# Kernel tuning notes

Measured on AMD Instinct MI355X. Metric: run time of the kernel, lower is better.

Reference implementation:

```python
import jax, jax.numpy as jnp
import numpy as np

M_IND = 1024   # inducing points
K_NN = 16      # nearest neighbors
JITTER = 1e-4


def rbf(X, Z):
    # unit-variance, unit-lengthscale RBF kernel; returns (K, squared distances)
    sq = jnp.sum(X * X, -1)[:, None] + jnp.sum(Z * Z, -1)[None, :] - 2.0 * (X @ Z.T)
    sq = jnp.maximum(sq, 0.0)
    return jnp.exp(-0.5 * sq), sq


def setup_inputs() -> dict:
    key = jax.random.key(0)
    k1, k2, k3 = jax.random.split(key, 3)
    return {
        "X": jax.random.normal(k1, (65536, 3), jnp.float32),
        "Z": jax.random.normal(k2, (M_IND, 3), jnp.float32),
        "Lu_raw": jax.random.normal(k3, (M_IND, M_IND), jnp.float32),
        "mu": jnp.zeros((M_IND,), jnp.float32),
    }


def reference(X, Z, Lu_raw, mu):
    N = X.shape[0]
    Kxx = jnp.ones((N,), X.dtype)                      # diag of RBF(X,X) is 1
    Kxz, dist = rbf(X, Z)                              # [N,M], [N,M]
    Kzz, _ = rbf(Z, Z)                                 # [M,M]

    # transform_to(lower_cholesky): strict lower triangle + exp(diag)
    Lu = jnp.tril(Lu_raw, -1) + jnp.diag(jnp.exp(jnp.diag(Lu_raw)))

    eyeM = jnp.eye(M_IND, dtype=X.dtype)
    L = jnp.linalg.cholesky(Kzz + JITTER * eyeM)       # [M,M]
    Kzz_j = L @ L.T                                    # == little_L @ little_L.T math (Kzz + jitter*I)
    Su = Lu @ Lu.T                                     # full variational covariance

    # K nearest inducing points per data point (argsort(dist)[:, :K])
    _, idx = jax.lax.top_k(-dist, K_NN)                # [N,K]

    lKzz = Kzz_j[idx[:, :, None], idx[:, None, :]]     # [N,K,K] gathered submatrices
    lS = Su[idx[:, :, None], idx[:, None, :]]          # [N,K,K]
    lKxz = jnp.take_along_axis(Kxz, idx, axis=1)       # [N,K]
    lmu = mu[idx]                                      # [N,K]

    eyeK = jnp.eye(K_NN, dtype=X.dtype)
    inv = jnp.linalg.inv(lKzz + JITTER * eyeK)         # batched tiny inverses [N,K,K]
    W = jnp.einsum('nk,nkj->nj', lKxz, inv)            # [N,K]

    mean = jnp.einsum('nk,nk->n', W, lmu)              # [N]
    cov = (Kxx
           - jnp.einsum('ni,nij,nj->n', W, lKzz, W)
           + jnp.einsum('ni,nij,nj->n', W, lS, W))
    std = jnp.sqrt(jnp.clip(cov, 0.05, None))          # qF scale = clamp(cov, 0.05)**0.5
    return jnp.stack([mean, std])                      # [2,N] qF parameters
```

## Files before the change

### kernel.cpp

```cpp
#include <hip/hip_runtime.h>
#include <math.h>

#define N_PTS 65536
#define M_IND 1024
#define KNN 16
#define JITTER 1e-4f

#define PACKED_FLOATS (M_IND * (M_IND + 1) / 2)
#define PACKED_BYTES  ((size_t)PACKED_FLOATS * sizeof(float))

#define TSU 32
#define SU_BLOCKS 528
#define PTS_PER_BLK 128
#define QSTRIDE 17
#define GRID_BLKS (N_PTS / PTS_PER_BLK)


__device__ __forceinline__ void su_tile(const float* __restrict__ Lu_raw,
                                        float* __restrict__ P,
                                        int bid, int tid,
                                        float (*As)[36], float (*Bs)[36]) {
    int rt = (int)((sqrtf(8.0f * (float)bid + 1.0f) - 1.0f) * 0.5f);
    while ((rt + 1) * (rt + 2) / 2 <= bid) ++rt;
    while (rt * (rt + 1) / 2 > bid) --rt;
    int ct = bid - rt * (rt + 1) / 2;
    int i0 = rt * TSU, j0 = ct * TSU;

    int tx = tid & 15, ty = tid >> 4;
    int sr = tid >> 3, sc = (tid & 7) << 2;
    float a00 = 0.f, a01 = 0.f, a10 = 0.f, a11 = 0.f;

    int nch = ct + 1;
    int gi = i0 + sr, gj = j0 + sr;
    float4 pa = *(const float4*)(Lu_raw + (unsigned)gi * M_IND + sc);
    float4 pb = *(const float4*)(Lu_raw + (unsigned)gj * M_IND + sc);

    for (int c = 0; c < nch; ++c) {
        int gk = (c << 5) + sc;
        float aa[4] = {pa.x, pa.y, pa.z, pa.w};
        float bb[4] = {pb.x, pb.y, pb.z, pb.w};
        #pragma unroll
        for (int q = 0; q < 4; ++q) {
            int k = gk + q;
            aa[q] = (k < gi) ? aa[q] : ((k == gi) ? __expf(aa[q]) : 0.0f);
            bb[q] = (k < gj) ? bb[q] : ((k == gj) ? __expf(bb[q]) : 0.0f);
        }
        *(float4*)&As[sr][sc] = make_float4(aa[0], aa[1], aa[2], aa[3]);
        *(float4*)&Bs[sr][sc] = make_float4(bb[0], bb[1], bb[2], bb[3]);
        __syncthreads();
        if (c + 1 < nch) {
            int kn = ((c + 1) << 5) + sc;
            pa = *(const float4*)(Lu_raw + (unsigned)gi * M_IND + kn);
            pb = *(const float4*)(Lu_raw + (unsigned)gj * M_IND + kn);
        }
        #pragma unroll
        for (int kk = 0; kk < 32; kk += 4) {
            float4 av0 = *(const float4*)&As[ty][kk];
            float4 av1 = *(const float4*)&As[ty + 16][kk];
            float4 bv0 = *(const float4*)&Bs[tx][kk];
            float4 bv1 = *(const float4*)&Bs[tx + 16][kk];
            a00 = fmaf(av0.x, bv0.x, fmaf(av0.y, bv0.y, fmaf(av0.z, bv0.z, fmaf(av0.w, bv0.w, a00))));
            a01 = fmaf(av0.x, bv1.x, fmaf(av0.y, bv1.y, fmaf(av0.z, bv1.z, fmaf(av0.w, bv1.w, a01))));
            a10 = fmaf(av1.x, bv0.x, fmaf(av1.y, bv0.y, fmaf(av1.z, bv0.z, fmaf(av1.w, bv0.w, a10))));
            a11 = fmaf(av1.x, bv1.x, fmaf(av1.y, bv1.y, fmaf(av1.z, bv1.z, fmaf(av1.w, bv1.w, a11))));
        }
        __syncthreads();
    }

    int ia = i0 + ty, ib = i0 + ty + 16;
    int ja = j0 + tx, jb = j0 + tx + 16;
    if (ja <= ia) P[((unsigned)ia * (ia + 1) >> 1) + ja] = a00;
    if (jb <= ia) P[((unsigned)ia * (ia + 1) >> 1) + jb] = a01;
    if (ja <= ib) P[((unsigned)ib * (ib + 1) >> 1) + ja] = a10;
    if (jb <= ib) P[((unsigned)ib * (ib + 1) >> 1) + jb] = a11;
}

__global__ __launch_bounds__(256) void su_kernel(const float* __restrict__ Lu_raw,
                                                 float* __restrict__ P) {
    __shared__ float As[TSU][36];
    __shared__ float Bs[TSU][36];
    su_tile(Lu_raw, P, blockIdx.x, threadIdx.x, As, Bs);
}

__device__ __forceinline__ void ce(unsigned long long& x, unsigned long long& y) {
    unsigned long long a = x, b = y;
    bool c = a < b;
    x = c ? a : b;
    y = c ? b : a;
}
__device__ __forceinline__ void ce(float& x, float& y) {
    float a = fminf(x, y), b = fmaxf(x, y);
    x = a; y = b;
}

template <typename KT>
__device__ __forceinline__ void sort16(KT* a) {
    #pragma unroll
    for (int p = 1; p < 16; p <<= 1)
        #pragma unroll
        for (int k = p; k >= 1; k >>= 1)
            #pragma unroll
            for (int j = k & (p - 1); j + k < 16; j += 2 * k)
                #pragma unroll
                for (int i = 0; i < k; ++i)
                    if (i + j + k < 16)
                        if (((i + j) / (2 * p)) == ((i + j + k) / (2 * p)))
                            ce(a[i + j], a[i + j + k]);
}

template <typename KT>
__device__ __forceinline__ void cleanup16(KT* a) {
    #pragma unroll
    for (int d = 8; d >= 1; d >>= 1)
        #pragma unroll
        for (int i = 0; i < 16; ++i)
            if ((i & d) == 0) ce(a[i], a[i | d]);
}

__device__ __forceinline__ float uval(float4 z, float xn0, float xn1, float xn2) {
    return fmaf(xn0, z.x, fmaf(xn1, z.y, fmaf(xn2, z.z, z.w)));
}

template <int MODE>
__global__ __launch_bounds__(256, 2) void vnngp_kernel(const float* __restrict__ X,
                                                       const float* __restrict__ Z,
                                                       const float* __restrict__ mu,
                                                       float* __restrict__ P,
                                                       const float* __restrict__ Lu_raw,
                                                       unsigned int* __restrict__ ctr,
                                                       float* __restrict__ out) {
    __shared__ __align__(16) char smem[37888];
    float4* Zs = (float4*)smem;
    float* mus = (float*)(smem + 16384);
    unsigned long long* qb = (unsigned long long*)(smem + 20480);
    int tid = threadIdx.x;

    for (int r = tid; r < M_IND; r += 256) {
        float zx = Z[r * 3 + 0], zy = Z[r * 3 + 1], zz = Z[r * 3 + 2];
        Zs[r] = make_float4(zx, zy, zz, 0.5f * (zx * zx + zy * zy + zz * zz));
        mus[r] = mu[r];
    }

    if (MODE == 2) {
        float (*As)[36] = (float (*)[36])(smem + 20480);
        float (*Bs)[36] = (float (*)[36])(smem + 20480 + 4608);
        int t = blockIdx.x;
        #pragma unroll
        for (int r = 16; r < 32; ++r) {
            int s = (r * (r + 1)) >> 1;
            if (t >= s) ++t;
        }
        su_tile(Lu_raw, P, t, tid, As, Bs);
        if (blockIdx.x < 16) {
            int r = 16 + blockIdx.x;
            su_tile(Lu_raw, P, (r * (r + 1)) >> 1, tid, As, Bs);
        }
        __syncthreads();
        if (tid == 0) {
            __threadfence();
            atomicAdd(ctr, 1u);
        }
    } else {
        __syncthreads();
    }

    {
        int pt = tid >> 2, sub = tid & 3;
        int nA = blockIdx.x * PTS_PER_BLK + pt;
        int nB = nA + 64;
        float xA0 = X[nA * 3 + 0], xA1 = X[nA * 3 + 1], xA2 = X[nA * 3 + 2];
        float xB0 = X[nB * 3 + 0], xB1 = X[nB * 3 + 1], xB2 = X[nB * 3 + 2];
        float xqA = fmaf(xA0, xA0, fmaf(xA1, xA1, xA2 * xA2));
        float xqB = fmaf(xB0, xB0, fmaf(xB1, xB1, xB2 * xB2));
        float nA0 = -xA0, nA1 = -xA1, nA2 = -xA2;
        float nB0 = -xB0, nB1 = -xB1, nB2 = -xB2;
        int mbase = sub << 8;
        int rot = sub << 1;

        float TA[16], TB[16];
        #pragma unroll
        for (int j = 0; j < 16; ++j) { TA[j] = 3.4e38f; TB[j] = 3.4e38f; }
        #pragma unroll 1
        for (int c = 0; c < 16; ++c) {
            int base = mbase + (c << 4);
            #pragma unroll
            for (int j = 0; j < 16; ++j) {
                int m = base + ((j + rot) & 15);
                float4 z = Zs[m];
                TA[j] = fminf(TA[j], uval(z, nA0, nA1, nA2));
                TB[j] = fminf(TB[j], uval(z, nB0, nB1, nB2));
            }
        }
        sort16(TA);
        sort16(TB);
        #pragma unroll
        for (int round = 1; round <= 2; round <<= 1) {
            float oA[16], oB[16];
            #pragma unroll
            for (int i = 0; i < 16; ++i) {
                oA[i] = __shfl_xor(TA[i], round, 64);
                oB[i] = __shfl_xor(TB[i], round, 64);
            }
            #pragma unroll
            for (int i = 0; i < 16; ++i) {
                TA[i] = fminf(TA[i], oA[15 - i]);
                TB[i] = fminf(TB[i], oB[15 - i]);
            }
            cleanup16(TA);
            cleanup16(TB);
        }
        float TstarA = TA[15], TstarB = TB[15];

        unsigned short* mycA = ((unsigned short*)qb) + pt * (QSTRIDE * 4) + sub * 16;
        unsigned short* mycB = ((unsigned short*)qb) + (pt + 64) * (QSTRIDE * 4) + sub * 16;
        int cntA = 0, cntB = 0;
        #pragma unroll 1
        for (int c = 0; c < 16; ++c) {
            int base = mbase + (c << 4);
            #pragma unroll
            for (int j = 0; j < 16; ++j) {
                int m = base + ((j + rot) & 15);
                float4 z = Zs[m];
                float uA = uval(z, nA0, nA1, nA2);
                float uB = uval(z, nB0, nB1, nB2);
                if (uA <= TstarA) { if (cntA < 16) mycA[cntA] = (unsigned short)m; ++cntA; }
                if (uB <= TstarB) { if (cntB < 16) mycB[cntB] = (unsigned short)m; ++cntB; }
            }
        }

        int ovfA = cntA > 16 ? 1 : 0;
        ovfA |= __shfl_xor(ovfA, 1, 64);
        ovfA |= __shfl_xor(ovfA, 2, 64);
        int ovfB = cntB > 16 ? 1 : 0;
        ovfB |= __shfl_xor(ovfB, 1, 64);
        ovfB |= __shfl_xor(ovfB, 2, 64);

        if (!ovfA) {
            const unsigned long long* m64 = (const unsigned long long*)mycA;
            unsigned long long raw[4] = {m64[0], m64[1], m64[2], m64[3]};
            unsigned long long C[16];
            #pragma unroll
            for (int i = 0; i < 16; ++i) {
                int m = (int)((raw[i >> 2] >> ((i & 3) * 16)) & 0x3FF);
                float u = uval(Zs[m], nA0, nA1, nA2);
                float d = fmaxf(fmaf(2.0f, u, xqA), 0.0f);
                unsigned long long key =
                    ((unsigned long long)__float_as_uint(d) << 32) | (unsigned)m;
                C[i] = (i < cntA) ? key : ~0ULL;
            }
            sort16(C);
            #pragma unroll
            for (int round = 1; round <= 2; round <<= 1) {
                unsigned long long o[16];
                #pragma unroll
                for (int i = 0; i < 16; ++i) o[i] = __shfl_xor(C[i], round, 64);
                #pragma unroll
                for (int i = 0; i < 16; ++i) {
                    unsigned long long b = o[15 - i];
                    C[i] = C[i] < b ? C[i] : b;
                }
                cleanup16(C);
            }
            if (sub == 0) {
                #pragma unroll
                for (int i = 0; i < 16; ++i) qb[pt * QSTRIDE + i] = C[i];
            }
        } else if (sub == 0) {
            unsigned long long R[16];
            #pragma unroll
            for (int i = 0; i < 16; ++i) R[i] = ~0ULL;
            for (int m = 0; m < M_IND; ++m) {
                float u = uval(Zs[m], nA0, nA1, nA2);
                float d = fmaxf(fmaf(2.0f, u, xqA), 0.0f);
                unsigned long long kk =
                    ((unsigned long long)__float_as_uint(d) << 32) | (unsigned)m;
                if (kk < R[15]) {
                    #pragma unroll
                    for (int j = 0; j < 16; ++j) {
                        unsigned long long t = R[j];
                        bool cc = kk < t;
                        R[j] = cc ? kk : t;
                        kk = cc ? t : kk;
                    }
                }
            }
            #pragma unroll
            for (int i = 0; i < 16; ++i) qb[pt * QSTRIDE + i] = R[i];
        }

        if (!ovfB) {
            const unsigned long long* m64 = (const unsigned long long*)mycB;
            unsigned long long raw[4] = {m64[0], m64[1], m64[2], m64[3]};
            unsigned long long C[16];
            #pragma unroll
            for (int i = 0; i < 16; ++i) {
                int m = (int)((raw[i >> 2] >> ((i & 3) * 16)) & 0x3FF);
                float u = uval(Zs[m], nB0, nB1, nB2);
                float d = fmaxf(fmaf(2.0f, u, xqB), 0.0f);
                unsigned long long key =
                    ((unsigned long long)__float_as_uint(d) << 32) | (unsigned)m;
                C[i] = (i < cntB) ? key : ~0ULL;
            }
            sort16(C);
            #pragma unroll
            for (int round = 1; round <= 2; round <<= 1) {
                unsigned long long o[16];
                #pragma unroll
                for (int i = 0; i < 16; ++i) o[i] = __shfl_xor(C[i], round, 64);
                #pragma unroll
                for (int i = 0; i < 16; ++i) {
                    unsigned long long b = o[15 - i];
                    C[i] = C[i] < b ? C[i] : b;
                }
                cleanup16(C);
            }
            if (sub == 0) {
                #pragma unroll
                for (int i = 0; i < 16; ++i) qb[(pt + 64) * QSTRIDE + i] = C[i];
            }
        } else if (sub == 0) {
            unsigned long long R[16];
            #pragma unroll
            for (int i = 0; i < 16; ++i) R[i] = ~0ULL;
            for (int m = 0; m < M_IND; ++m) {
                float u = uval(Zs[m], nB0, nB1, nB2);
                float d = fmaxf(fmaf(2.0f, u, xqB), 0.0f);
                unsigned long long kk =
                    ((unsigned long long)__float_as_uint(d) << 32) | (unsigned)m;
                if (kk < R[15]) {
                    #pragma unroll
                    for (int j = 0; j < 16; ++j) {
                        unsigned long long t = R[j];
                        bool cc = kk < t;
                        R[j] = cc ? kk : t;
                        kk = cc ? t : kk;
                    }
                }
            }
            #pragma unroll
            for (int i = 0; i < 16; ++i) qb[(pt + 64) * QSTRIDE + i] = R[i];
        }
    }
    __syncthreads();

    if (MODE == 2) {
        if (tid == 0) {
            while (__hip_atomic_load(ctr, __ATOMIC_ACQUIRE, __HIP_MEMORY_SCOPE_AGENT)
                   < (unsigned)GRID_BLKS)
                __builtin_amdgcn_s_sleep(8);
        }
        __syncthreads();
    }
    if (tid >= PTS_PER_BLK) return;

    int n = blockIdx.x * PTS_PER_BLK + tid;
    int idx[KNN];
    float kv[KNN];
    float nx[KNN], ny[KNN], nz[KNN], nq[KNN];
    #pragma unroll
    for (int a = 0; a < KNN; ++a) {
        unsigned long long k = qb[tid * QSTRIDE + a];
        idx[a] = (int)(k & 0xFFFFFFFFULL);
        float d = __uint_as_float((unsigned)(k >> 32));
        kv[a] = __expf(-0.5f * d);
        float4 z = Zs[idx[a]];
        nx[a] = z.x; ny[a] = z.y; nz[a] = z.z; nq[a] = z.w;
    }

    float A[KNN * (KNN + 1) / 2];
    #pragma unroll
    for (int r = 0; r < KNN; ++r) {
        A[r * (r + 1) / 2 + r] = 1.0f + 2.0f * JITTER;
        #pragma unroll
        for (int c = 0; c < r; ++c) {
            float dot = fmaf(nx[r], nx[c], fmaf(ny[r], ny[c], nz[r] * nz[c]));
            A[r * (r + 1) / 2 + c] = __expf(fminf(dot - nq[r] - nq[c], 0.0f));
        }
    }

    #pragma unroll
    for (int c = 0; c < KNN; ++c) {
        float diag = A[c * (c + 1) / 2 + c];
        #pragma unroll
        for (int k = 0; k < c; ++k) {
            float l = A[c * (c + 1) / 2 + k];
            diag = fmaf(-l, l, diag);
        }
        float rinv = __frsqrt_rn(fmaxf(diag, 1e-12f));
        A[c * (c + 1) / 2 + c] = rinv;
        #pragma unroll
        for (int r = c + 1; r < KNN; ++r) {
            float v = A[r * (r + 1) / 2 + c];
            #pragma unroll
            for (int k = 0; k < c; ++k)
                v = fmaf(-A[r * (r + 1) / 2 + k], A[c * (c + 1) / 2 + k], v);
            A[r * (r + 1) / 2 + c] = v * rinv;
        }
    }

    float w[KNN];
    #pragma unroll
    for (int r = 0; r < KNN; ++r) {
        float v = kv[r];
        #pragma unroll
        for (int c = 0; c < r; ++c) v = fmaf(-A[r * (r + 1) / 2 + c], w[c], v);
        w[r] = v * A[r * (r + 1) / 2 + r];
    }
    #pragma unroll
    for (int r = KNN - 1; r >= 0; --r) {
        float v = w[r];
        #pragma unroll
        for (int c = r + 1; c < KNN; ++c) v = fmaf(-A[c * (c + 1) / 2 + r], w[c], v);
        w[r] = v * A[r * (r + 1) / 2 + r];
    }

    float wk = 0.f, ww = 0.f, mean = 0.f;
    #pragma unroll
    for (int a = 0; a < KNN; ++a) {
        wk = fmaf(w[a], kv[a], wk);
        ww = fmaf(w[a], w[a], ww);
        mean = fmaf(w[a], mus[idx[a]], mean);
    }

    float qs = 0.f;
    if (MODE != 0) {
        #pragma unroll
        for (int r = 0; r < KNN; ++r) {
            int a = idx[r];
            float wr = w[r];
            float rowacc = 0.f;
            #pragma unroll
            for (int c = 0; c < r; ++c) {
                int b = idx[c];
                int hi = a > b ? a : b;
                int lo = a > b ? b : a;
                rowacc = fmaf(w[c], P[((unsigned)hi * (hi + 1) >> 1) + lo], rowacc);
            }
            qs = fmaf(wr, fmaf(wr, P[((unsigned)a * (a + 1) >> 1) + a], 2.0f * rowacc), qs);
        }
    } else {
        int si[KNN]; float sw[KNN];
        #pragma unroll
        for (int a = 0; a < KNN; ++a) { si[a] = idx[a]; sw[a] = w[a]; }
        #pragma unroll
        for (int a = 1; a < KNN; ++a) {
            int iv = si[a]; float wv = sw[a];
            int b = a - 1;
            while (b >= 0 && si[b] > iv) { si[b + 1] = si[b]; sw[b + 1] = sw[b]; --b; }
            si[b + 1] = iv; sw[b + 1] = wv;
        }
        int s = 0;
        int kend = si[KNN - 1];
        for (int k = 0; k <= kend; ++k) {
            float v = 0.f;
            if (s < KNN && si[s] == k) {
                v = sw[s] * __expf(Lu_raw[(unsigned)k * M_IND + k]);
                ++s;
            }
            for (int a = s; a < KNN; ++a)
                v = fmaf(sw[a], Lu_raw[(unsigned)si[a] * M_IND + k], v);
            qs = fmaf(v, v, qs);
        }
    }

    float cov = 1.0f - (wk - JITTER * ww) + qs;
    float sd = sqrtf(fmaxf(cov, 0.05f));
    out[n] = mean;
    out[N_PTS + n] = sd;
}

extern "C" void kernel_launch(void* const* d_in, const int* in_sizes, int n_in,
                              void* d_out, int out_size, void* d_ws, size_t ws_size,
                              hipStream_t stream) {
    const float* X      = (const float*)d_in[0];
    const float* Z      = (const float*)d_in[1];
    const float* Lu_raw = (const float*)d_in[2];
    const float* mu     = (const float*)d_in[3];
    float* out = (float*)d_out;

    if (ws_size >= PACKED_BYTES + 64) {
        float* P = (float*)d_ws;
        unsigned int* ctr = (unsigned int*)((char*)d_ws + PACKED_BYTES);
        hipMemsetAsync(ctr, 0, sizeof(unsigned int), stream);
        vnngp_kernel<2><<<GRID_BLKS, 256, 0, stream>>>(X, Z, mu, P, Lu_raw, ctr, out);
    } else if (ws_size >= PACKED_BYTES) {
        float* P = (float*)d_ws;
        su_kernel<<<SU_BLOCKS, 256, 0, stream>>>(Lu_raw, P);
        vnngp_kernel<1><<<GRID_BLKS, 256, 0, stream>>>(X, Z, mu, P, Lu_raw, nullptr, out);
    } else {
        vnngp_kernel<0><<<GRID_BLKS, 256, 0, stream>>>(X, Z, mu, nullptr, Lu_raw, nullptr, out);
    }
}
```

Baseline: 163.0 us.

## Split fused kernel into kNN selection and Cholesky solve kernels via workspace

Adds a two-kernel path used when the workspace is large enough. The first kernel computes the packed Su tiles and a threshold-based top-16 neighbor selection, writing (distance, index) keys to global memory. The second kernel rebuilds the 16x16 Kzz submatrix, solves it with an in-register Cholesky, and splits the Su quadratic form across two threads per point. This removes the global counter synchronisation and the mixed workload of the fused kernel, at the cost of an extra launch and an 8 MB global round trip for the neighbor keys.

Result: slower. 173.8 us (+6.7%).

```diff
diff --git a/kernel.cpp b/kernel.cpp
--- a/kernel.cpp
+++ b/kernel.cpp
@@ -8,6 +8,7 @@
 
 #define PACKED_FLOATS (M_IND * (M_IND + 1) / 2)
 #define PACKED_BYTES  ((size_t)PACKED_FLOATS * sizeof(float))
+#define QBG_BYTES     ((size_t)N_PTS * KNN * 8)
 
 #define TSU 32
 #define SU_BLOCKS 528
@@ -119,6 +120,255 @@
 
 __device__ __forceinline__ float uval(float4 z, float xn0, float xn1, float xn2) {
     return fmaf(xn0, z.x, fmaf(xn1, z.y, fmaf(xn2, z.z, z.w)));
+}
+
+__global__ __launch_bounds__(256, 2) void sel_kernel(const float* __restrict__ X,
+                                                     const float* __restrict__ Z,
+                                                     float* __restrict__ P,
+                                                     const float* __restrict__ Lu_raw,
+                                                     unsigned long long* __restrict__ qbg) {
+    __shared__ __align__(16) char smem[25600];
+    float4* Zs = (float4*)smem;
+    unsigned long long* qb = (unsigned long long*)(smem + 16384);
+    int tid = threadIdx.x;
+
+    for (int r = tid; r < M_IND; r += 256) {
+        float zx = Z[r * 3 + 0], zy = Z[r * 3 + 1], zz = Z[r * 3 + 2];
+        Zs[r] = make_float4(zx, zy, zz, 0.5f * (zx * zx + zy * zy + zz * zz));
+    }
+
+    if (blockIdx.x < SU_BLOCKS) {
+        float (*As)[36] = (float (*)[36])(smem + 16384);
+        float (*Bs)[36] = (float (*)[36])(smem + 16384 + 4608);
+        su_tile(Lu_raw, P, blockIdx.x, tid, As, Bs);
+    } else {
+        __syncthreads();
+    }
+
+    int pt = tid >> 2, sub = tid & 3;
+    int n = blockIdx.x * 64 + pt;
+    float x0 = X[n * 3 + 0], x1 = X[n * 3 + 1], x2 = X[n * 3 + 2];
+    float xq = fmaf(x0, x0, fmaf(x1, x1, x2 * x2));
+    float xn0 = -x0, xn1 = -x1, xn2 = -x2;
+    int mbase = sub << 8;
+    int rot = sub << 1;
+
+    float T[16];
+    #pragma unroll
+    for (int j = 0; j < 16; ++j) T[j] = 3.4e38f;
+    #pragma unroll 1
+    for (int c = 0; c < 16; ++c) {
+        int base = mbase + (c << 4);
+        #pragma unroll
+        for (int j = 0; j < 16; ++j) {
+            int m = base + ((j + rot) & 15);
+            float4 z = Zs[m];
+            T[j] = fminf(T[j], uval(z, xn0, xn1, xn2));
+        }
+    }
+    sort16(T);
+    #pragma unroll
+    for (int round = 1; round <= 2; round <<= 1) {
+        float o[16];
+        #pragma unroll
+        for (int i = 0; i < 16; ++i) o[i] = __shfl_xor(T[i], round, 64);
+        #pragma unroll
+        for (int i = 0; i < 16; ++i) T[i] = fminf(T[i], o[15 - i]);
+        cleanup16(T);
+    }
+    float Tstar = T[15];
+
+    unsigned short* myc = ((unsigned short*)qb) + pt * (QSTRIDE * 4) + sub * 16;
+    int cnt = 0;
+    #pragma unroll 1
+    for (int c = 0; c < 16; ++c) {
+        int base = mbase + (c << 4);
+        #pragma unroll
+        for (int j = 0; j < 16; ++j) {
+            int m = base + ((j + rot) & 15);
+            float4 z = Zs[m];
+            float u = uval(z, xn0, xn1, xn2);
+            if (u <= Tstar) { if (cnt < 16) myc[cnt] = (unsigned short)m; ++cnt; }
+        }
+    }
+
+    int ovf = cnt > 16 ? 1 : 0;
+    ovf |= __shfl_xor(ovf, 1, 64);
+    ovf |= __shfl_xor(ovf, 2, 64);
+
+    unsigned long long* kout = qbg + (size_t)n * KNN;
+
+    if (!ovf) {
+        const unsigned long long* m64 = (const unsigned long long*)myc;
+        unsigned long long raw[4] = {m64[0], m64[1], m64[2], m64[3]};
+        unsigned long long C[16];
+        #pragma unroll
+        for (int i = 0; i < 16; ++i) {
+            int m = (int)((raw[i >> 2] >> ((i & 3) * 16)) & 0x3FF);
+            float u = uval(Zs[m], xn0, xn1, xn2);
+            float d = fmaxf(fmaf(2.0f, u, xq), 0.0f);
+            unsigned long long key =
+                ((unsigned long long)__float_as_uint(d) << 32) | (unsigned)m;
+            C[i] = (i < cnt) ? key : ~0ULL;
+        }
+        sort16(C);
+        #pragma unroll
+        for (int round = 1; round <= 2; round <<= 1) {
+            unsigned long long o[16];
+            #pragma unroll
+            for (int i = 0; i < 16; ++i) o[i] = __shfl_xor(C[i], round, 64);
+            #pragma unroll
+            for (int i = 0; i < 16; ++i) {
+                unsigned long long b = o[15 - i];
+                C[i] = C[i] < b ? C[i] : b;
+            }
+            cleanup16(C);
+        }
+        if (sub == 0) {
+            #pragma unroll
+            for (int i = 0; i < 16; ++i) kout[i] = C[i];
+        }
+    } else if (sub == 0) {
+        unsigned long long R[16];
+        #pragma unroll
+        for (int i = 0; i < 16; ++i) R[i] = ~0ULL;
+        for (int m = 0; m < M_IND; ++m) {
+            float u = uval(Zs[m], xn0, xn1, xn2);
+            float d = fmaxf(fmaf(2.0f, u, xq), 0.0f);
+            unsigned long long kk =
+                ((unsigned long long)__float_as_uint(d) << 32) | (unsigned)m;
+            if (kk < R[15]) {
+                #pragma unroll
+                for (int j = 0; j < 16; ++j) {
+                    unsigned long long t = R[j];
+                    bool cc = kk < t;
+                    R[j] = cc ? kk : t;
+                    kk = cc ? t : kk;
+                }
+            }
+        }
+        #pragma unroll
+        for (int i = 0; i < 16; ++i) kout[i] = R[i];
+    }
+}
+
+__global__ __launch_bounds__(128, 2) void p2_kernel(const float* __restrict__ Z,
+                                                    const float* __restrict__ mu,
+                                                    const float* __restrict__ P,
+                                                    const unsigned long long* __restrict__ qbg,
+                                                    float* __restrict__ out) {
+    __shared__ __align__(16) char smem[20992];
+    float4* Zs = (float4*)smem;
+    float* mus = (float*)(smem + 16384);
+    float* xch = (float*)(smem + 20480);
+    int tid = threadIdx.x;
+
+    for (int r = tid; r < M_IND; r += 128) {
+        float zx = Z[r * 3 + 0], zy = Z[r * 3 + 1], zz = Z[r * 3 + 2];
+        Zs[r] = make_float4(zx, zy, zz, 0.5f * (zx * zx + zy * zy + zz * zz));
+        mus[r] = mu[r];
+    }
+    __syncthreads();
+
+    int role = tid >> 6;
+    int pt = tid & 63;
+    int n = blockIdx.x * 64 + pt;
+
+    int idx[KNN];
+    float kv[KNN];
+    float nx[KNN], ny[KNN], nz[KNN], nq[KNN];
+    const unsigned long long* kp = qbg + (size_t)n * KNN;
+    #pragma unroll
+    for (int a = 0; a < KNN; ++a) {
+        unsigned long long k = kp[a];
+        idx[a] = (int)(k & 0xFFFFFFFFULL);
+        float d = __uint_as_float((unsigned)(k >> 32));
+        kv[a] = __expf(-0.5f * d);
+        float4 z = Zs[idx[a]];
+        nx[a] = z.x; ny[a] = z.y; nz[a] = z.z; nq[a] = z.w;
+    }
+
+    float A[KNN * (KNN + 1) / 2];
+    #pragma unroll
+    for (int r = 0; r < KNN; ++r) {
+        A[r * (r + 1) / 2 + r] = 1.0f + 2.0f * JITTER;
+        #pragma unroll
+        for (int c = 0; c < r; ++c) {
+            float dot = fmaf(nx[r], nx[c], fmaf(ny[r], ny[c], nz[r] * nz[c]));
+            A[r * (r + 1) / 2 + c] = __expf(fminf(dot - nq[r] - nq[c], 0.0f));
+        }
+    }
+
+    #pragma unroll
+    for (int c = 0; c < KNN; ++c) {
+        float diag = A[c * (c + 1) / 2 + c];
+        #pragma unroll
+        for (int k = 0; k < c; ++k) {
+            float l = A[c * (c + 1) / 2 + k];
+            diag = fmaf(-l, l, diag);
+        }
+        float rinv = __frsqrt_rn(fmaxf(diag, 1e-12f));
+        A[c * (c + 1) / 2 + c] = rinv;
+        #pragma unroll
+        for (int r = c + 1; r < KNN; ++r) {
+            float v = A[r * (r + 1) / 2 + c];
+            #pragma unroll
+            for (int k = 0; k < c; ++k)
+                v = fmaf(-A[r * (r + 1) / 2 + k], A[c * (c + 1) / 2 + k], v);
+            A[r * (r + 1) / 2 + c] = v * rinv;
+        }
+    }
+
+    float w[KNN];
+    #pragma unroll
+    for (int r = 0; r < KNN; ++r) {
+        float v = kv[r];
+        #pragma unroll
+        for (int c = 0; c < r; ++c) v = fmaf(-A[r * (r + 1) / 2 + c], w[c], v);
+        w[r] = v * A[r * (r + 1) / 2 + r];
+    }
+    #pragma unroll
+    for (int r = KNN - 1; r >= 0; --r) {
+        float v = w[r];
+        #pragma unroll
+        for (int c = r + 1; c < KNN; ++c) v = fmaf(-A[c * (c + 1) / 2 + r], w[c], v);
+        w[r] = v * A[r * (r + 1) / 2 + r];
+    }
+
+    float wk = 0.f, ww = 0.f, mean = 0.f;
+    #pragma unroll
+    for (int a = 0; a < KNN; ++a) {
+        wk = fmaf(w[a], kv[a], wk);
+        ww = fmaf(w[a], w[a], ww);
+        mean = fmaf(w[a], mus[idx[a]], mean);
+    }
+
+    float qs_p = 0.f;
+    #pragma unroll
+    for (int r = 0; r < KNN; ++r) {
+        if ((r & 1) == role) {
+            int a = idx[r];
+            float wr = w[r];
+            float rowacc = 0.f;
+            #pragma unroll
+            for (int c = 0; c < r; ++c) {
+                int b = idx[c];
+                int hi = a > b ? a : b;
+                int lo = a > b ? b : a;
+                rowacc = fmaf(w[c], P[((unsigned)hi * (hi + 1) >> 1) + lo], rowacc);
+            }
+            qs_p = fmaf(wr, fmaf(wr, P[((unsigned)a * (a + 1) >> 1) + a], 2.0f * rowacc), qs_p);
+        }
+    }
+    xch[tid] = qs_p;
+    __syncthreads();
+    if (role == 0) {
+        float qs = qs_p + xch[tid + 64];
+        float cov = 1.0f - (wk - JITTER * ww) + qs;
+        float sd = sqrtf(fmaxf(cov, 0.05f));
+        out[n] = mean;
+        out[N_PTS + n] = sd;
+    }
 }
 
 template <int MODE>
@@ -478,7 +728,12 @@
     const float* mu     = (const float*)d_in[3];
     float* out = (float*)d_out;
 
-    if (ws_size >= PACKED_BYTES + 64) {
+    if (ws_size >= PACKED_BYTES + QBG_BYTES) {
+        float* P = (float*)d_ws;
+        unsigned long long* qbg = (unsigned long long*)((char*)d_ws + PACKED_BYTES);
+        sel_kernel<<<N_PTS / 64, 256, 0, stream>>>(X, Z, P, Lu_raw, qbg);
+        p2_kernel<<<N_PTS / 64, 128, 0, stream>>>(Z, mu, P, qbg, out);
+    } else if (ws_size >= PACKED_BYTES + 64) {
         float* P = (float*)d_ws;
         unsigned int* ctr = (unsigned int*)((char*)d_ws + PACKED_BYTES);
         hipMemsetAsync(ctr, 0, sizeof(unsigned int), stream);
```

## Split per-point 16x16 Cholesky solve across four lanes with shuffles

Applied to the files above, without the earlier changes.

In the packed-Su modes, each point's 16x16 Cholesky, triangular solves and quadratic form are now spread over a quad of four lanes, each owning four rows in a cyclic layout. Columns and partial sums move between lanes with wavefront shuffles. All 256 threads now do this phase instead of half of them idling, and per-thread register pressure drops. The cost is many shuffle operations and serial dependence through the column loop.

New measurement: 176.0 us. 1.08x slower.

```diff
diff --git a/kernel.cpp b/kernel.cpp
--- a/kernel.cpp
+++ b/kernel.cpp
@@ -120,6 +120,10 @@
 __device__ __forceinline__ float uval(float4 z, float xn0, float xn1, float xn2) {
     return fmaf(xn0, z.x, fmaf(xn1, z.y, fmaf(xn2, z.z, z.w)));
 }
+
+#define LI0(c) ((c) & 3)
+#define LI1(c) ((c) & 7)
+#define LI2(c) ((c) < 12 ? (c) : 0)
 
 template <int MODE>
 __global__ __launch_bounds__(256, 2) void vnngp_kernel(const float* __restrict__ X,
@@ -351,122 +355,299 @@
         }
         __syncthreads();
     }
-    if (tid >= PTS_PER_BLK) return;
-
-    int n = blockIdx.x * PTS_PER_BLK + tid;
-    int idx[KNN];
-    float kv[KNN];
-    float nx[KNN], ny[KNN], nz[KNN], nq[KNN];
-    #pragma unroll
-    for (int a = 0; a < KNN; ++a) {
-        unsigned long long k = qb[tid * QSTRIDE + a];
-        idx[a] = (int)(k & 0xFFFFFFFFULL);
-        float d = __uint_as_float((unsigned)(k >> 32));
-        kv[a] = __expf(-0.5f * d);
-        float4 z = Zs[idx[a]];
-        nx[a] = z.x; ny[a] = z.y; nz[a] = z.z; nq[a] = z.w;
-    }
-
-    float A[KNN * (KNN + 1) / 2];
-    #pragma unroll
-    for (int r = 0; r < KNN; ++r) {
-        A[r * (r + 1) / 2 + r] = 1.0f + 2.0f * JITTER;
-        #pragma unroll
-        for (int c = 0; c < r; ++c) {
-            float dot = fmaf(nx[r], nx[c], fmaf(ny[r], ny[c], nz[r] * nz[c]));
-            A[r * (r + 1) / 2 + c] = __expf(fminf(dot - nq[r] - nq[c], 0.0f));
-        }
-    }
-
-    #pragma unroll
-    for (int c = 0; c < KNN; ++c) {
-        float diag = A[c * (c + 1) / 2 + c];
-        #pragma unroll
-        for (int k = 0; k < c; ++k) {
-            float l = A[c * (c + 1) / 2 + k];
-            diag = fmaf(-l, l, diag);
-        }
-        float rinv = __frsqrt_rn(fmaxf(diag, 1e-12f));
-        A[c * (c + 1) / 2 + c] = rinv;
-        #pragma unroll
-        for (int r = c + 1; r < KNN; ++r) {
-            float v = A[r * (r + 1) / 2 + c];
-            #pragma unroll
-            for (int k = 0; k < c; ++k)
-                v = fmaf(-A[r * (r + 1) / 2 + k], A[c * (c + 1) / 2 + k], v);
-            A[r * (r + 1) / 2 + c] = v * rinv;
-        }
-    }
-
-    float w[KNN];
-    #pragma unroll
-    for (int r = 0; r < KNN; ++r) {
-        float v = kv[r];
-        #pragma unroll
-        for (int c = 0; c < r; ++c) v = fmaf(-A[r * (r + 1) / 2 + c], w[c], v);
-        w[r] = v * A[r * (r + 1) / 2 + r];
-    }
-    #pragma unroll
-    for (int r = KNN - 1; r >= 0; --r) {
-        float v = w[r];
-        #pragma unroll
-        for (int c = r + 1; c < KNN; ++c) v = fmaf(-A[c * (c + 1) / 2 + r], w[c], v);
-        w[r] = v * A[r * (r + 1) / 2 + r];
-    }
-
-    float wk = 0.f, ww = 0.f, mean = 0.f;
-    #pragma unroll
-    for (int a = 0; a < KNN; ++a) {
-        wk = fmaf(w[a], kv[a], wk);
-        ww = fmaf(w[a], w[a], ww);
-        mean = fmaf(w[a], mus[idx[a]], mean);
-    }
-
-    float qs = 0.f;
-    if (MODE != 0) {
+
+    if (MODE == 0) {
+        if (tid >= PTS_PER_BLK) return;
+        int n = blockIdx.x * PTS_PER_BLK + tid;
+        int idx[KNN];
+        float kv[KNN];
+        float nx[KNN], ny[KNN], nz[KNN], nq[KNN];
+        #pragma unroll
+        for (int a = 0; a < KNN; ++a) {
+            unsigned long long k = qb[tid * QSTRIDE + a];
+            idx[a] = (int)(k & 0xFFFFFFFFULL);
+            float d = __uint_as_float((unsigned)(k >> 32));
+            kv[a] = __expf(-0.5f * d);
+            float4 z = Zs[idx[a]];
+            nx[a] = z.x; ny[a] = z.y; nz[a] = z.z; nq[a] = z.w;
+        }
+
+        float A[KNN * (KNN + 1) / 2];
         #pragma unroll
         for (int r = 0; r < KNN; ++r) {
-            int a = idx[r];
-            float wr = w[r];
-            float rowacc = 0.f;
+            A[r * (r + 1) / 2 + r] = 1.0f + 2.0f * JITTER;
             #pragma unroll
             for (int c = 0; c < r; ++c) {
-                int b = idx[c];
-                int hi = a > b ? a : b;
-                int lo = a > b ? b : a;
-                rowacc = fmaf(w[c], P[((unsigned)hi * (hi + 1) >> 1) + lo], rowacc);
-            }
-            qs = fmaf(wr, fmaf(wr, P[((unsigned)a * (a + 1) >> 1) + a], 2.0f * rowacc), qs);
-        }
-    } else {
-        int si[KNN]; float sw[KNN];
-        #pragma unroll
-        for (int a = 0; a < KNN; ++a) { si[a] = idx[a]; sw[a] = w[a]; }
-        #pragma unroll
-        for (int a = 1; a < KNN; ++a) {
-            int iv = si[a]; float wv = sw[a];
-            int b = a - 1;
-            while (b >= 0 && si[b] > iv) { si[b + 1] = si[b]; sw[b + 1] = sw[b]; --b; }
-            si[b + 1] = iv; sw[b + 1] = wv;
-        }
-        int s = 0;
-        int kend = si[KNN - 1];
-        for (int k = 0; k <= kend; ++k) {
-            float v = 0.f;
-            if (s < KNN && si[s] == k) {
-                v = sw[s] * __expf(Lu_raw[(unsigned)k * M_IND + k]);
-                ++s;
-            }
-            for (int a = s; a < KNN; ++a)
-                v = fmaf(sw[a], Lu_raw[(unsigned)si[a] * M_IND + k], v);
-            qs = fmaf(v, v, qs);
-        }
-    }
-
-    float cov = 1.0f - (wk - JITTER * ww) + qs;
-    float sd = sqrtf(fmaxf(cov, 0.05f));
-    out[n] = mean;
-    out[N_PTS + n] = sd;
+                float dot = fmaf(nx[r], nx[c], fmaf(ny[r], ny[c], nz[r] * nz[c]));
+                A[r * (r + 1) / 2 + c] = __expf(fminf(dot - nq[r] - nq[c], 0.0f));
+            }
+        }
+
+        #pragma unroll
+        for (int c = 0; c < KNN; ++c) {
+            float diag = A[c * (c + 1) / 2 + c];
+            #pragma unroll
+            for (int k = 0; k < c; ++k) {
+                float lv = A[c * (c + 1) / 2 + k];
+                diag = fmaf(-lv, lv, diag);
+            }
+            float rinv = __frsqrt_rn(fmaxf(diag, 1e-12f));
+            A[c * (c + 1) / 2 + c] = rinv;
+            #pragma unroll
+            for (int r = c + 1; r < KNN; ++r) {
+                float v = A[r * (r + 1) / 2 + c];
+                #pragma unroll
+                for (int k = 0; k < c; ++k)
+                    v = fmaf(-A[r * (r + 1) / 2 + k], A[c * (c + 1) / 2 + k], v);
+                A[r * (r + 1) / 2 + c] = v * rinv;
+            }
+        }
+
+        float w[KNN];
+        #pragma unroll
+        for (int r = 0; r < KNN; ++r) {
+            float v = kv[r];
+            #pragma unroll
+            for (int c = 0; c < r; ++c) v = fmaf(-A[r * (r + 1) / 2 + c], w[c], v);
+            w[r] = v * A[r * (r + 1) / 2 + r];
+        }
+        #pragma unroll
+        for (int r = KNN - 1; r >= 0; --r) {
+            float v = w[r];
+            #pragma unroll
+            for (int c = r + 1; c < KNN; ++c) v = fmaf(-A[c * (c + 1) / 2 + r], w[c], v);
+            w[r] = v * A[r * (r + 1) / 2 + r];
+        }
+
+        float wk = 0.f, ww = 0.f, mean = 0.f;
+        #pragma unroll
+        for (int a = 0; a < KNN; ++a) {
+            wk = fmaf(w[a], kv[a], wk);
+            ww = fmaf(w[a], w[a], ww);
+            mean = fmaf(w[a], mus[idx[a]], mean);
+        }
+
+        float qs = 0.f;
+        {
+            int si[KNN]; float sw[KNN];
+            #pragma unroll
+            for (int a = 0; a < KNN; ++a) { si[a] = idx[a]; sw[a] = w[a]; }
+            #pragma unroll
+            for (int a = 1; a < KNN; ++a) {
+                int iv = si[a]; float wv = sw[a];
+                int b = a - 1;
+                while (b >= 0 && si[b] > iv) { si[b + 1] = si[b]; sw[b + 1] = sw[b]; --b; }
+                si[b + 1] = iv; sw[b + 1] = wv;
+            }
+            int s = 0;
+            int kend = si[KNN - 1];
+            for (int k = 0; k <= kend; ++k) {
+                float v = 0.f;
+                if (s < KNN && si[s] == k) {
+                    v = sw[s] * __expf(Lu_raw[(unsigned)k * M_IND + k]);
+                    ++s;
+                }
+                for (int a = s; a < KNN; ++a)
+                    v = fmaf(sw[a], Lu_raw[(unsigned)si[a] * M_IND + k], v);
+                qs = fmaf(v, v, qs);
+            }
+        }
+
+        float cov = 1.0f - (wk - JITTER * ww) + qs;
+        float sd = sqrtf(fmaxf(cov, 0.05f));
+        out[n] = mean;
+        out[N_PTS + n] = sd;
+        return;
+    }
+
+    {
+        int l = tid & 3;
+        int lanebase = (tid & 63) & ~3;
+
+        #pragma unroll 1
+        for (int b = 0; b < 2; ++b) {
+            int g = (tid >> 2) + (b << 6);
+            int n = blockIdx.x * PTS_PER_BLK + g;
+
+            int idx[16];
+            int iown[4];
+            float kvown[4];
+            float4 zrown[4];
+            #pragma unroll
+            for (int a = 0; a < 16; ++a) {
+                unsigned long long k = qb[g * QSTRIDE + a];
+                int ia = (int)(k & 0xFFFFFFFFULL);
+                float d = __uint_as_float((unsigned)(k >> 32));
+                float kva = __expf(-0.5f * d);
+                idx[a] = ia;
+                if ((a & 3) == l) {
+                    iown[a >> 2] = ia;
+                    kvown[a >> 2] = kva;
+                    zrown[a >> 2] = Zs[ia];
+                }
+            }
+
+            float L0[4], L1[8], L2[12], L3[16];
+            float dg[4];
+            #pragma unroll
+            for (int k = 0; k < 4; ++k) dg[k] = 1.0f + 2.0f * JITTER;
+            #pragma unroll
+            for (int c = 0; c < 16; ++c) {
+                float4 zc = Zs[idx[c]];
+                #pragma unroll
+                for (int k = 0; k < 4; ++k) {
+                    if (c < 4 * (k + 1)) {
+                        int r = l + 4 * k;
+                        float dot = fmaf(zrown[k].x, zc.x,
+                                    fmaf(zrown[k].y, zc.y, zrown[k].z * zc.z));
+                        float val = __expf(fminf(dot - zrown[k].w - zc.w, 0.0f));
+                        if (c < r) {
+                            if (k == 0) L0[LI0(c)] = val;
+                            else if (k == 1) L1[LI1(c)] = val;
+                            else if (k == 2) L2[LI2(c)] = val;
+                            else L3[c] = val;
+                        }
+                    }
+                }
+            }
+
+            float rinvown[4];
+            #pragma unroll
+            for (int c = 0; c < 16; ++c) {
+                const int owner = c & 3, kc = c >> 2;
+                float dval = __shfl(dg[kc], lanebase + owner, 64);
+                float rinv = __frsqrt_rn(fmaxf(dval, 1e-12f));
+                if (l == owner) rinvown[kc] = rinv;
+                float cv[4];
+                #pragma unroll
+                for (int k = 0; k < 4; ++k) {
+                    cv[k] = 0.f;
+                    if (c < 4 * (k + 1)) {
+                        int r = l + 4 * k;
+                        if (r > c) {
+                            float v;
+                            if (k == 0) { v = L0[LI0(c)] * rinv; L0[LI0(c)] = v; }
+                            else if (k == 1) { v = L1[LI1(c)] * rinv; L1[LI1(c)] = v; }
+                            else if (k == 2) { v = L2[LI2(c)] * rinv; L2[LI2(c)] = v; }
+                            else { v = L3[c] * rinv; L3[c] = v; }
+                            cv[k] = v;
+                        }
+                    }
+                }
+                #pragma unroll
+                for (int j = c + 1; j < 16; ++j) {
+                    float colj = __shfl(cv[j >> 2], lanebase + (j & 3), 64);
+                    #pragma unroll
+                    for (int k = 0; k < 4; ++k) {
+                        if (j < 4 * (k + 1)) {
+                            int r = l + 4 * k;
+                            if (r > j) {
+                                float u = cv[k] * colj;
+                                if (k == 0) L0[LI0(j)] -= u;
+                                else if (k == 1) L1[LI1(j)] -= u;
+                                else if (k == 2) L2[LI2(j)] -= u;
+                                else L3[j] -= u;
+                            } else if (r == j) {
+                                dg[k] = fmaf(-colj, colj, dg[k]);
+                            }
+                        }
+                    }
+                }
+            }
+
+            float acc[4];
+            #pragma unroll
+            for (int k = 0; k < 4; ++k) acc[k] = kvown[k];
+            float yown[4];
+            #pragma unroll
+            for (int r = 0; r < 16; ++r) {
+                const int owner = r & 3, kr = r >> 2;
+                float yr = __shfl(acc[kr] * rinvown[kr], lanebase + owner, 64);
+                if (l == owner) yown[kr] = yr;
+                #pragma unroll
+                for (int k = 0; k < 4; ++k) {
+                    if (r < 4 * (k + 1)) {
+                        int rr = l + 4 * k;
+                        if (rr > r) {
+                            float lv;
+                            if (k == 0) lv = L0[LI0(r)];
+                            else if (k == 1) lv = L1[LI1(r)];
+                            else if (k == 2) lv = L2[LI2(r)];
+                            else lv = L3[r];
+                            acc[k] = fmaf(-lv, yr, acc[k]);
+                        }
+                    }
+                }
+            }
+
+            float wfull[16];
+            float wown[4] = {0.f, 0.f, 0.f, 0.f};
+            #pragma unroll
+            for (int r = 15; r >= 0; --r) {
+                const int owner = r & 3, kr = r >> 2;
+                float contrib = 0.f;
+                #pragma unroll
+                for (int k = 0; k < 4; ++k) {
+                    if (r < 4 * (k + 1)) {
+                        int j = l + 4 * k;
+                        if (j > r) {
+                            float lv;
+                            if (k == 0) lv = L0[LI0(r)];
+                            else if (k == 1) lv = L1[LI1(r)];
+                            else if (k == 2) lv = L2[LI2(r)];
+                            else lv = L3[r];
+                            contrib = fmaf(lv, wown[k], contrib);
+                        }
+                    }
+                }
+                contrib += __shfl_xor(contrib, 1, 64);
+                contrib += __shfl_xor(contrib, 2, 64);
+                float wr = __shfl((yown[kr] - contrib) * rinvown[kr],
+                                  lanebase + owner, 64);
+                wfull[r] = wr;
+                if (l == owner) wown[kr] = wr;
+            }
+
+            float wkp = 0.f, wwp = 0.f, mnp = 0.f;
+            #pragma unroll
+            for (int k = 0; k < 4; ++k) {
+                wkp = fmaf(wown[k], kvown[k], wkp);
+                wwp = fmaf(wown[k], wown[k], wwp);
+                mnp = fmaf(wown[k], mus[iown[k]], mnp);
+            }
+
+            float qsp = 0.f;
+            #pragma unroll
+            for (int k = 0; k < 4; ++k) {
+                int r = l + 4 * k;
+                int a = iown[k];
+                float wr = wown[k];
+                float rowacc = 0.f;
+                #pragma unroll
+                for (int c = 0; c < 15; ++c) {
+                    if (c < r) {
+                        int bb2 = idx[c];
+                        int hi = a > bb2 ? a : bb2;
+                        int lo = a > bb2 ? bb2 : a;
+                        rowacc = fmaf(wfull[c], P[((unsigned)hi * (hi + 1) >> 1) + lo], rowacc);
+                    }
+                }
+                qsp = fmaf(wr, fmaf(wr, P[((unsigned)a * (a + 1) >> 1) + a], 2.0f * rowacc), qsp);
+            }
+
+            wkp += __shfl_xor(wkp, 1, 64); wkp += __shfl_xor(wkp, 2, 64);
+            wwp += __shfl_xor(wwp, 1, 64); wwp += __shfl_xor(wwp, 2, 64);
+            mnp += __shfl_xor(mnp, 1, 64); mnp += __shfl_xor(mnp, 2, 64);
+            qsp += __shfl_xor(qsp, 1, 64); qsp += __shfl_xor(qsp, 2, 64);
+
+            if (l == 0) {
+                float cov = 1.0f - (wkp - JITTER * wwp) + qsp;
+                float sd = sqrtf(fmaxf(cov, 0.05f));
+                out[n] = mnp;
+                out[N_PTS + n] = sd;
+            }
+        }
+    }
 }
 
 extern "C" void kernel_launch(void* const* d_in, const int* in_sizes, int n_in,
```

## Drop fused Su grid-barrier mode and move Cholesky scratch to shared memory

Applied to the files above, without the earlier changes.

Removes the single-launch mode that computed the packed Su tiles inside the main kernel and spin-waited on a global atomic counter. Instead, a separate su_kernel launch precedes the main kernel. The per-thread 136-float Cholesky matrix moves from registers into a padded shared-memory slab, which grows LDS to about 80KB and likely cuts register pressure. The risk is an extra kernel launch, added LDS traffic, and lower occupancy from the larger shared footprint.

After: 182.2 us. 11.8% more time.

```diff
diff --git a/kernel.cpp b/kernel.cpp
--- a/kernel.cpp
+++ b/kernel.cpp
@@ -127,9 +127,8 @@
                                                        const float* __restrict__ mu,
                                                        float* __restrict__ P,
                                                        const float* __restrict__ Lu_raw,
-                                                       unsigned int* __restrict__ ctr,
                                                        float* __restrict__ out) {
-    __shared__ __align__(16) char smem[37888];
+    __shared__ __align__(16) char smem[81408];
     float4* Zs = (float4*)smem;
     float* mus = (float*)(smem + 16384);
     unsigned long long* qb = (unsigned long long*)(smem + 20480);
@@ -140,29 +139,7 @@
         Zs[r] = make_float4(zx, zy, zz, 0.5f * (zx * zx + zy * zy + zz * zz));
         mus[r] = mu[r];
     }
-
-    if (MODE == 2) {
-        float (*As)[36] = (float (*)[36])(smem + 20480);
-        float (*Bs)[36] = (float (*)[36])(smem + 20480 + 4608);
-        int t = blockIdx.x;
-        #pragma unroll
-        for (int r = 16; r < 32; ++r) {
-            int s = (r * (r + 1)) >> 1;
-            if (t >= s) ++t;
-        }
-        su_tile(Lu_raw, P, t, tid, As, Bs);
-        if (blockIdx.x < 16) {
-            int r = 16 + blockIdx.x;
-            su_tile(Lu_raw, P, (r * (r + 1)) >> 1, tid, As, Bs);
-        }
-        __syncthreads();
-        if (tid == 0) {
-            __threadfence();
-            atomicAdd(ctr, 1u);
-        }
-    } else {
-        __syncthreads();
-    }
+    __syncthreads();
 
     {
         int pt = tid >> 2, sub = tid & 3;
@@ -343,58 +320,54 @@
     }
     __syncthreads();
 
-    if (MODE == 2) {
-        if (tid == 0) {
-            while (__hip_atomic_load(ctr, __ATOMIC_ACQUIRE, __HIP_MEMORY_SCOPE_AGENT)
-                   < (unsigned)GRID_BLKS)
-                __builtin_amdgcn_s_sleep(8);
-        }
-        __syncthreads();
-    }
+    int idx[KNN];
+    float kv[KNN], musr[KNN];
+    float nx[KNN], ny[KNN], nz[KNN], nq[KNN];
+    if (tid < PTS_PER_BLK) {
+        #pragma unroll
+        for (int a = 0; a < KNN; ++a) {
+            unsigned long long k = qb[tid * QSTRIDE + a];
+            int ia = (int)(k & 0xFFFFFFFFULL);
+            float d = __uint_as_float((unsigned)(k >> 32));
+            idx[a] = ia;
+            kv[a] = __expf(-0.5f * d);
+            float4 z = Zs[ia];
+            nx[a] = z.x; ny[a] = z.y; nz[a] = z.z; nq[a] = z.w;
+            musr[a] = mus[ia];
+        }
+    }
+    __syncthreads();
     if (tid >= PTS_PER_BLK) return;
 
-    int n = blockIdx.x * PTS_PER_BLK + tid;
-    int idx[KNN];
-    float kv[KNN];
-    float nx[KNN], ny[KNN], nz[KNN], nq[KNN];
-    #pragma unroll
-    for (int a = 0; a < KNN; ++a) {
-        unsigned long long k = qb[tid * QSTRIDE + a];
-        idx[a] = (int)(k & 0xFFFFFFFFULL);
-        float d = __uint_as_float((unsigned)(k >> 32));
-        kv[a] = __expf(-0.5f * d);
-        float4 z = Zs[idx[a]];
-        nx[a] = z.x; ny[a] = z.y; nz[a] = z.z; nq[a] = z.w;
-    }
-
-    float A[KNN * (KNN + 1) / 2];
+    float* Ab = (float*)(smem + 11264) + tid * 137;
+
     #pragma unroll
     for (int r = 0; r < KNN; ++r) {
-        A[r * (r + 1) / 2 + r] = 1.0f + 2.0f * JITTER;
+        Ab[r * (r + 1) / 2 + r] = 1.0f + 2.0f * JITTER;
         #pragma unroll
         for (int c = 0; c < r; ++c) {
             float dot = fmaf(nx[r], nx[c], fmaf(ny[r], ny[c], nz[r] * nz[c]));
-            A[r * (r + 1) / 2 + c] = __expf(fminf(dot - nq[r] - nq[c], 0.0f));
+            Ab[r * (r + 1) / 2 + c] = __expf(fminf(dot - nq[r] - nq[c], 0.0f));
         }
     }
 
     #pragma unroll
     for (int c = 0; c < KNN; ++c) {
-        float diag = A[c * (c + 1) / 2 + c];
+        float diag = Ab[c * (c + 1) / 2 + c];
         #pragma unroll
         for (int k = 0; k < c; ++k) {
-            float l = A[c * (c + 1) / 2 + k];
-            diag = fmaf(-l, l, diag);
+            float lv = Ab[c * (c + 1) / 2 + k];
+            diag = fmaf(-lv, lv, diag);
         }
         float rinv = __frsqrt_rn(fmaxf(diag, 1e-12f));
-        A[c * (c + 1) / 2 + c] = rinv;
+        Ab[c * (c + 1) / 2 + c] = rinv;
         #pragma unroll
         for (int r = c + 1; r < KNN; ++r) {
-            float v = A[r * (r + 1) / 2 + c];
+            float v = Ab[r * (r + 1) / 2 + c];
             #pragma unroll
             for (int k = 0; k < c; ++k)
-                v = fmaf(-A[r * (r + 1) / 2 + k], A[c * (c + 1) / 2 + k], v);
-            A[r * (r + 1) / 2 + c] = v * rinv;
+                v = fmaf(-Ab[r * (r + 1) / 2 + k], Ab[c * (c + 1) / 2 + k], v);
+            Ab[r * (r + 1) / 2 + c] = v * rinv;
         }
     }
 
@@ -403,15 +376,15 @@
     for (int r = 0; r < KNN; ++r) {
         float v = kv[r];
         #pragma unroll
-        for (int c = 0; c < r; ++c) v = fmaf(-A[r * (r + 1) / 2 + c], w[c], v);
-        w[r] = v * A[r * (r + 1) / 2 + r];
+        for (int c = 0; c < r; ++c) v = fmaf(-Ab[r * (r + 1) / 2 + c], w[c], v);
+        w[r] = v * Ab[r * (r + 1) / 2 + r];
     }
     #pragma unroll
     for (int r = KNN - 1; r >= 0; --r) {
         float v = w[r];
         #pragma unroll
-        for (int c = r + 1; c < KNN; ++c) v = fmaf(-A[c * (c + 1) / 2 + r], w[c], v);
-        w[r] = v * A[r * (r + 1) / 2 + r];
+        for (int c = r + 1; c < KNN; ++c) v = fmaf(-Ab[c * (c + 1) / 2 + r], w[c], v);
+        w[r] = v * Ab[r * (r + 1) / 2 + r];
     }
 
     float wk = 0.f, ww = 0.f, mean = 0.f;
@@ -419,7 +392,7 @@
     for (int a = 0; a < KNN; ++a) {
         wk = fmaf(w[a], kv[a], wk);
         ww = fmaf(w[a], w[a], ww);
-        mean = fmaf(w[a], mus[idx[a]], mean);
+        mean = fmaf(w[a], musr[a], mean);
     }
 
     float qs = 0.f;
@@ -463,6 +436,7 @@
         }
     }
 
+    int n = blockIdx.x * PTS_PER_BLK + tid;
     float cov = 1.0f - (wk - JITTER * ww) + qs;
     float sd = sqrtf(fmaxf(cov, 0.05f));
     out[n] = mean;
@@ -478,16 +452,11 @@
     const float* mu     = (const float*)d_in[3];
     float* out = (float*)d_out;
 
-    if (ws_size >= PACKED_BYTES + 64) {
-        float* P = (float*)d_ws;
-        unsigned int* ctr = (unsigned int*)((char*)d_ws + PACKED_BYTES);
-        hipMemsetAsync(ctr, 0, sizeof(unsigned int), stream);
-        vnngp_kernel<2><<<GRID_BLKS, 256, 0, stream>>>(X, Z, mu, P, Lu_raw, ctr, out);
-    } else if (ws_size >= PACKED_BYTES) {
+    if (ws_size >= PACKED_BYTES) {
         float* P = (float*)d_ws;
         su_kernel<<<SU_BLOCKS, 256, 0, stream>>>(Lu_raw, P);
-        vnngp_kernel<1><<<GRID_BLKS, 256, 0, stream>>>(X, Z, mu, P, Lu_raw, nullptr, out);
+        vnngp_kernel<1><<<GRID_BLKS, 256, 0, stream>>>(X, Z, mu, P, Lu_raw, out);
     } else {
-        vnngp_kernel<0><<<GRID_BLKS, 256, 0, stream>>>(X, Z, mu, nullptr, Lu_raw, nullptr, out);
-    }
-}
+        vnngp_kernel<0><<<GRID_BLKS, 256, 0, stream>>>(X, Z, mu, nullptr, Lu_raw, out);
+    }
+}
```
